# Performance work log

Hardware: AMD Instinct MI355X
Metric: run time of the kernel (lower is better)

## Reference

```python
import jax, jax.numpy as jnp
import numpy as np
import math

B, S, E, H = 4, 1024, 1024, 16
D = E // H


def setup_inputs() -> dict:
    key = jax.random.key(0)
    ks = jax.random.split(key, 10)
    inp = {
        "query": jax.random.normal(ks[0], (B, S, E), dtype=jnp.float32),
        "key": jax.random.normal(ks[1], (B, S, E), dtype=jnp.float32),
        "value": jax.random.normal(ks[2], (B, S, E), dtype=jnp.float32),
        "attn_mask": jax.random.randint(ks[3], (B * H, S, S), 0, 2).astype(bool),
        "key_padding_mask": jax.random.randint(ks[4], (B, S), 0, 2).astype(bool),
        # nn.Linear(E, E, bias=False) weights, stored [out, in] as in torch
        "Wq": jax.random.normal(ks[5], (E, E), dtype=jnp.float32) * 0.02,
        "Wk": jax.random.normal(ks[6], (E, E), dtype=jnp.float32) * 0.02,
        "Wv": jax.random.normal(ks[7], (E, E), dtype=jnp.float32) * 0.02,
        "Wo": jax.random.normal(ks[8], (E, E), dtype=jnp.float32) * 0.02,
    }
    return inp


def reference(query, key, value, attn_mask, key_padding_mask, Wq, Wk, Wv, Wo):
    # projections: torch Linear => x @ W.T; split heads -> [B,H,S,D]
    Q = (query @ Wq.T).reshape(B, S, H, D).transpose(0, 2, 1, 3)
    K = (key @ Wk.T).reshape(B, S, H, D).transpose(0, 2, 1, 3)
    V = (value @ Wv.T).reshape(B, S, H, D).transpose(0, 2, 1, 3)

    scores = jnp.einsum('bhid,bhkd->bhik', Q, K) / math.sqrt(D)  # [B,H,S,S]

    am = attn_mask.reshape(B, H, S, S)
    kpm = jnp.broadcast_to(key_padding_mask[:, None, None, :], (B, H, S, S))
    mask = am | kpm

    # faithful quirks: masked scores set to 0 (not -inf); softmax over dim=2
    # (the QUERY axis i of [b,h,i,k]); masked weights zeroed after softmax.
    scores = jnp.where(mask, 0.0, scores)
    weights = jax.nn.softmax(scores, axis=2)
    weights = jnp.where(mask, 0.0, weights)

    attn = jnp.einsum('bhij,bhjk->bhik', weights, V)  # [B,H,S,D]
    attn = attn.transpose(0, 2, 1, 3).reshape(B, S, H * D)
    return attn @ Wo.T
```

## Files before the change

### kernel.cpp

```cpp
#include <hip/hip_runtime.h>
#include <stdint.h>

#define S_ 1024
#define E_ 1024
#define H_ 16
#define D_ 64
#define BH_ 64

typedef __attribute__((ext_vector_type(4))) float f32x4;
typedef __attribute__((ext_vector_type(8))) _Float16 f16x8;

__device__ __forceinline__ void gl_lds16(const void* g, void* l) {
  __builtin_amdgcn_global_load_lds((__attribute__((address_space(1))) void*)(g),
                                   (__attribute__((address_space(3))) void*)(l), 16, 0, 0);
}

__global__ __launch_bounds__(256) void cvt_f16(const float* __restrict__ q,
                                               const float* __restrict__ k,
                                               const float* __restrict__ v,
                                               const float* __restrict__ wq,
                                               const float* __restrict__ wk,
                                               const float* __restrict__ wv,
                                               const float* __restrict__ wo,
                                               _Float16* __restrict__ dst) {
  size_t i = ((size_t)blockIdx.x * 256 + threadIdx.x) * 4;
  const size_t M4 = 4u << 20, M1 = 1u << 20;
  const float* src;
  size_t off;
  if (i < M4) { src = q; off = i; }
  else if (i < 2 * M4) { src = k; off = i - M4; }
  else if (i < 3 * M4) { src = v; off = i - 2 * M4; }
  else if (i < 3 * M4 + M1) { src = wq; off = i - 3 * M4; }
  else if (i < 3 * M4 + 2 * M1) { src = wk; off = i - (3 * M4 + M1); }
  else if (i < 3 * M4 + 3 * M1) { src = wv; off = i - (3 * M4 + 2 * M1); }
  else { src = wo; off = i - (3 * M4 + 3 * M1); }
  float4 f = *reinterpret_cast<const float4*>(src + off);
  _Float16 h[4];
  h[0] = (_Float16)f.x; h[1] = (_Float16)f.y; h[2] = (_Float16)f.z; h[3] = (_Float16)f.w;
  *reinterpret_cast<uint2*>(dst + i) = *reinterpret_cast<uint2*>(h);
}

__global__ __launch_bounds__(256) void pack_mask(const int* __restrict__ am,
                                                 const int* __restrict__ kpm,
                                                 uint32_t* __restrict__ mw) {
  size_t t = (size_t)blockIdx.x * 256 + threadIdx.x;
  size_t f = t * 4;
  int k = (int)(f & (S_ - 1));
  int b = (int)(f >> 24);
  int4 a = *reinterpret_cast<const int4*>(am + f);
  int4 kp = *reinterpret_cast<const int4*>(kpm + (size_t)b * S_ + k);
  uint32_t nib = (uint32_t)((a.x | kp.x) != 0) | ((uint32_t)((a.y | kp.y) != 0) << 1) |
                 ((uint32_t)((a.z | kp.z) != 0) << 2) | ((uint32_t)((a.w | kp.w) != 0) << 3);
  uint32_t v = nib << ((threadIdx.x & 7) * 4);
  v |= __shfl_xor(v, 1);
  v |= __shfl_xor(v, 2);
  v |= __shfl_xor(v, 4);
  if ((threadIdx.x & 7) == 0) mw[t >> 3] = v;
}

__global__ __launch_bounds__(256) void gemm_proj(const _Float16* __restrict__ qkv,
                                                 const _Float16* __restrict__ wts,
                                                 _Float16* __restrict__ QKo,
                                                 _Float16* __restrict__ Vt) {
  const int K = 1024, BM = 128, BK = 32;
  __shared__ __align__(16) _Float16 As[BM * BK];
  __shared__ __align__(16) _Float16 Bs[BM * BK];
  const int tid = threadIdx.x, wave = tid >> 6, lane = tid & 63;
  const int l15 = lane & 15, lk = lane >> 4;
  const int wr = wave >> 1, wc = wave & 1;
  const int mb = blockIdx.x, nb = blockIdx.y, z = blockIdx.z;
  const _Float16* A = qkv + (size_t)z * (4u << 20);
  const _Float16* Bw = wts + (size_t)z * (1u << 20);
  const int srow = (lane >> 2);
  const int scol = (lane & 3) * 8;
  f32x4 acc[4][4] = {};
  for (int kt = 0; kt < K / BK; ++kt) {
#pragma unroll
    for (int c = 0; c < 2; ++c) {
      int ch = wave * 2 + c;
      int row = ch * 16 + srow;
      gl_lds16(&A[(size_t)(mb * BM + row) * K + kt * BK + scol], &As[ch * 512]);
      gl_lds16(&Bw[(size_t)(nb * BM + row) * K + kt * BK + scol], &Bs[ch * 512]);
    }
    __syncthreads();
    f16x8 a[4], b[4];
#pragma unroll
    for (int m = 0; m < 4; ++m)
      a[m] = *reinterpret_cast<const f16x8*>(&As[(wr * 64 + m * 16 + l15) * BK + lk * 8]);
#pragma unroll
    for (int n = 0; n < 4; ++n)
      b[n] = *reinterpret_cast<const f16x8*>(&Bs[(wc * 64 + n * 16 + l15) * BK + lk * 8]);
#pragma unroll
    for (int m = 0; m < 4; ++m)
#pragma unroll
      for (int n = 0; n < 4; ++n)
        acc[m][n] = __builtin_amdgcn_mfma_f32_16x16x32_f16(a[m], b[n], acc[m][n], 0, 0, 0);
    __syncthreads();
  }
  const float qs = (z == 0) ? 0.125f : 1.0f;
#pragma unroll
  for (int m = 0; m < 4; ++m) {
#pragma unroll
    for (int n = 0; n < 4; ++n) {
#pragma unroll
      for (int r = 0; r < 4; ++r) {
        int gm = mb * BM + wr * 64 + m * 16 + lk * 4 + r;
        int gn = nb * BM + wc * 64 + n * 16 + l15;
        int bb = gm >> 10, s = gm & 1023, h = gn >> 6, d = gn & 63;
        int bh = bb * 16 + h;
        _Float16 v = (_Float16)(acc[m][n][r] * qs);
        if (z == 2)
          Vt[((size_t)bh * D_ + d) * S_ + s] = v;
        else
          QKo[(size_t)z * (4u << 20) + ((size_t)bh * S_ + s) * D_ + d] = v;
      }
    }
  }
}

__global__ __launch_bounds__(256) void attn_denom(const _Float16* __restrict__ Qh,
                                                  const _Float16* __restrict__ Kh,
                                                  const uint32_t* __restrict__ mw,
                                                  float* __restrict__ denom) {
  const int TI = 128, TK = 128, LD = 72;
  __shared__ __align__(16) _Float16 Qs[TI * LD];
  __shared__ __align__(16) _Float16 Ks[TK * LD];
  __shared__ uint32_t Ms[TI * 4];
  __shared__ float red[4][64];
  const int tid = threadIdx.x, wave = tid >> 6, lane = tid & 63;
  const int l15 = lane & 15, lk = lane >> 4;
  const int wr = wave >> 1, wc = wave & 1;
  const int bh = blockIdx.y, kb = blockIdx.x;
  const _Float16* Qb = Qh + (size_t)bh * S_ * D_;
  const _Float16* Kb = Kh + (size_t)bh * S_ * D_;
  const uint32_t* mrow = mw + (size_t)bh * S_ * 32;
#pragma unroll
  for (int j = 0; j < 4; ++j) {
    int c = tid + j * 256;
    int row = c >> 3, c8 = c & 7;
    *reinterpret_cast<uint4*>(&Ks[row * LD + c8 * 8]) =
        *reinterpret_cast<const uint4*>(&Kb[(size_t)(kb * TK + row) * D_ + c8 * 8]);
  }
  float csum[4] = {0.f, 0.f, 0.f, 0.f};
  for (int ib = 0; ib < S_ / TI; ++ib) {
    __syncthreads();
#pragma unroll
    for (int j = 0; j < 4; ++j) {
      int c = tid + j * 256;
      int row = c >> 3, c8 = c & 7;
      *reinterpret_cast<uint4*>(&Qs[row * LD + c8 * 8]) =
          *reinterpret_cast<const uint4*>(&Qb[(size_t)(ib * TI + row) * D_ + c8 * 8]);
    }
    Ms[tid] = mrow[(size_t)(ib * TI + (tid >> 2)) * 32 + kb * 4 + (tid & 3)];
    Ms[tid + 256] = mrow[(size_t)(ib * TI + 64 + (tid >> 2)) * 32 + kb * 4 + (tid & 3)];
    __syncthreads();
    f32x4 acc[4][4] = {};
#pragma unroll
    for (int kk = 0; kk < 2; ++kk) {
      f16x8 a[4], b[4];
#pragma unroll
      for (int m = 0; m < 4; ++m)
        a[m] = *reinterpret_cast<const f16x8*>(&Qs[(wr * 64 + m * 16 + l15) * LD + kk * 32 + lk * 8]);
#pragma unroll
      for (int n = 0; n < 4; ++n)
        b[n] = *reinterpret_cast<const f16x8*>(&Ks[(wc * 64 + n * 16 + l15) * LD + kk * 32 + lk * 8]);
#pragma unroll
      for (int m = 0; m < 4; ++m)
#pragma unroll
        for (int n = 0; n < 4; ++n)
          acc[m][n] = __builtin_amdgcn_mfma_f32_16x16x32_f16(a[m], b[n], acc[m][n], 0, 0, 0);
    }
#pragma unroll
    for (int n = 0; n < 4; ++n) {
      int kcol = wc * 64 + n * 16 + l15;
      int kwl = kcol >> 5;
      int kbit = kcol & 31;
      float part = 0.f;
#pragma unroll
      for (int m = 0; m < 4; ++m) {
        int lr0 = wr * 64 + m * 16 + lk * 4;
#pragma unroll
        for (int r = 0; r < 4; ++r) {
          bool msk = (Ms[(lr0 + r) * 4 + kwl] >> kbit) & 1;
          float e = __expf(acc[m][n][r]);
          part += msk ? 1.0f : e;
        }
      }
      csum[n] += part;
    }
  }
#pragma unroll
  for (int n = 0; n < 4; ++n) {
    float v = csum[n];
    v += __shfl_xor(v, 16);
    v += __shfl_xor(v, 32);
    csum[n] = v;
  }
  __syncthreads();
  if (lane < 16) {
#pragma unroll
    for (int n = 0; n < 4; ++n) red[wave][n * 16 + l15] = csum[n];
  }
  __syncthreads();
  if (tid < 128) {
    int wcx = tid >> 6, col = tid & 63;
    denom[(size_t)bh * S_ + kb * TK + wcx * 64 + col] = red[wcx][col] + red[wcx + 2][col];
  }
}

__global__ __launch_bounds__(256) void vscale(_Float16* __restrict__ Vt,
                                              const float* __restrict__ Dn) {
  size_t e = ((size_t)blockIdx.x * 256 + threadIdx.x) * 8;
  int bh = (int)(e >> 16);
  int s = (int)(e & (S_ - 1));
  uint4 raw = *reinterpret_cast<uint4*>(Vt + e);
  _Float16* h = reinterpret_cast<_Float16*>(&raw);
  const float* dp = Dn + (size_t)bh * S_ + s;
#pragma unroll
  for (int j = 0; j < 8; ++j) h[j] = (_Float16)((float)h[j] / dp[j]);
  *reinterpret_cast<uint4*>(Vt + e) = raw;
}

__global__ __launch_bounds__(256) void attn_pv(const _Float16* __restrict__ Qh,
                                               const _Float16* __restrict__ Kh,
                                               const _Float16* __restrict__ Vp,
                                               const uint32_t* __restrict__ mw,
                                               _Float16* __restrict__ An) {
  const int TI = 128, TK = 128, LD = 72, LW = 136;
  __shared__ __align__(16) _Float16 Qs[TI * LD];
  __shared__ __align__(16) _Float16 Ks[TK * LD];
  __shared__ __align__(16) _Float16 Ws[TI * LW];
  __shared__ uint32_t Ms[TI * 4];
  const int tid = threadIdx.x, wave = tid >> 6, lane = tid & 63;
  const int l15 = lane & 15, lk = lane >> 4;
  const int wr = wave >> 1, wc = wave & 1;
  const int bh = blockIdx.y, ib = blockIdx.x;
  const _Float16* Qb = Qh + (size_t)bh * S_ * D_;
  const _Float16* Kb = Kh + (size_t)bh * S_ * D_;
  const _Float16* Vb = Vp + ((size_t)bh << 16);
  const uint32_t* mrow = mw + (size_t)bh * S_ * 32;
#pragma unroll
  for (int j = 0; j < 4; ++j) {
    int c = tid + j * 256;
    int row = c >> 3, c8 = c & 7;
    *reinterpret_cast<uint4*>(&Qs[row * LD + c8 * 8]) =
        *reinterpret_cast<const uint4*>(&Qb[(size_t)(ib * TI + row) * D_ + c8 * 8]);
  }
  f32x4 acc2[4][2] = {};
  for (int kt = 0; kt < S_ / TK; ++kt) {
    __syncthreads();
#pragma unroll
    for (int j = 0; j < 4; ++j) {
      int c = tid + j * 256;
      int row = c >> 3, c8 = c & 7;
      *reinterpret_cast<uint4*>(&Ks[row * LD + c8 * 8]) =
          *reinterpret_cast<const uint4*>(&Kb[(size_t)(kt * TK + row) * D_ + c8 * 8]);
    }
    Ms[tid] = mrow[(size_t)(ib * TI + (tid >> 2)) * 32 + kt * 4 + (tid & 3)];
    Ms[tid + 256] = mrow[(size_t)(ib * TI + 64 + (tid >> 2)) * 32 + kt * 4 + (tid & 3)];
    __syncthreads();
    f32x4 acc[4][4] = {};
#pragma unroll
    for (int kk = 0; kk < 2; ++kk) {
      f16x8 a[4], b[4];
#pragma unroll
      for (int m = 0; m < 4; ++m)
        a[m] = *reinterpret_cast<const f16x8*>(&Qs[(wr * 64 + m * 16 + l15) * LD + kk * 32 + lk * 8]);
#pragma unroll
      for (int n = 0; n < 4; ++n)
        b[n] = *reinterpret_cast<const f16x8*>(&Ks[(wc * 64 + n * 16 + l15) * LD + kk * 32 + lk * 8]);
#pragma unroll
      for (int m = 0; m < 4; ++m)
#pragma unroll
        for (int n = 0; n < 4; ++n)
          acc[m][n] = __builtin_amdgcn_mfma_f32_16x16x32_f16(a[m], b[n], acc[m][n], 0, 0, 0);
    }
#pragma unroll
    for (int n = 0; n < 4; ++n) {
      int kcol = wc * 64 + n * 16 + l15;
      int kwl = kcol >> 5;
      int kbit = kcol & 31;
#pragma unroll
      for (int m = 0; m < 4; ++m) {
        int lr0 = wr * 64 + m * 16 + lk * 4;
#pragma unroll
        for (int r = 0; r < 4; ++r) {
          bool msk = (Ms[(lr0 + r) * 4 + kwl] >> kbit) & 1;
          float e = __expf(acc[m][n][r]);
          Ws[(lr0 + r) * LW + kcol] = msk ? (_Float16)0.f : (_Float16)e;
        }
      }
    }
    __syncthreads();
#pragma unroll
    for (int kk = 0; kk < 4; ++kk) {
      f16x8 a2[4], b2[2];
#pragma unroll
      for (int m = 0; m < 4; ++m)
        a2[m] = *reinterpret_cast<const f16x8*>(&Ws[(wr * 64 + m * 16 + l15) * LW + kk * 32 + lk * 8]);
#pragma unroll
      for (int n = 0; n < 2; ++n)
        b2[n] = *reinterpret_cast<const f16x8*>(
            &Vb[(size_t)(wc * 32 + n * 16 + l15) * S_ + kt * TK + kk * 32 + lk * 8]);
#pragma unroll
      for (int m = 0; m < 4; ++m)
#pragma unroll
        for (int n = 0; n < 2; ++n)
          acc2[m][n] = __builtin_amdgcn_mfma_f32_16x16x32_f16(a2[m], b2[n], acc2[m][n], 0, 0, 0);
    }
  }
  const int b_ = bh >> 4, h = bh & 15;
#pragma unroll
  for (int m = 0; m < 4; ++m) {
#pragma unroll
    for (int n = 0; n < 2; ++n) {
#pragma unroll
      for (int r = 0; r < 4; ++r) {
        int i = ib * TI + wr * 64 + m * 16 + lk * 4 + r;
        int d = wc * 32 + n * 16 + l15;
        An[((size_t)(b_ * S_ + i)) * E_ + h * D_ + d] = (_Float16)acc2[m][n][r];
      }
    }
  }
}

__global__ __launch_bounds__(256) void gemm_out(const _Float16* __restrict__ An,
                                               const _Float16* __restrict__ Bw,
                                               float* __restrict__ outp) {
  const int K = 1024, BM = 128, BN = 64, BK = 32;
  __shared__ __align__(16) _Float16 As[BM * BK];
  __shared__ __align__(16) _Float16 Bs[BN * BK];
  const int tid = threadIdx.x, wave = tid >> 6, lane = tid & 63;
  const int l15 = lane & 15, lk = lane >> 4;
  const int wr = wave >> 1, wc = wave & 1;
  const int mb = blockIdx.x, nb = blockIdx.y;
  const int srow = (lane >> 2), scol = (lane & 3) * 8;
  f32x4 acc[4][2] = {};
  for (int kt = 0; kt < K / BK; ++kt) {
#pragma unroll
    for (int c = 0; c < 2; ++c) {
      int ch = wave * 2 + c;
      int row = ch * 16 + srow;
      gl_lds16(&An[(size_t)(mb * BM + row) * K + kt * BK + scol], &As[ch * 512]);
    }
    {
      int row = wave * 16 + srow;
      gl_lds16(&Bw[(size_t)(nb * BN + row) * K + kt * BK + scol], &Bs[wave * 512]);
    }
    __syncthreads();
    f16x8 a[4], b[2];
#pragma unroll
    for (int m = 0; m < 4; ++m)
      a[m] = *reinterpret_cast<const f16x8*>(&As[(wr * 64 + m * 16 + l15) * BK + lk * 8]);
#pragma unroll
    for (int n = 0; n < 2; ++n)
      b[n] = *reinterpret_cast<const f16x8*>(&Bs[(wc * 32 + n * 16 + l15) * BK + lk * 8]);
#pragma unroll
    for (int m = 0; m < 4; ++m)
#pragma unroll
      for (int n = 0; n < 2; ++n)
        acc[m][n] = __builtin_amdgcn_mfma_f32_16x16x32_f16(a[m], b[n], acc[m][n], 0, 0, 0);
    __syncthreads();
  }
#pragma unroll
  for (int m = 0; m < 4; ++m) {
#pragma unroll
    for (int n = 0; n < 2; ++n) {
#pragma unroll
      for (int r = 0; r < 4; ++r) {
        int gm = mb * BM + wr * 64 + m * 16 + lk * 4 + r;
        int gn = nb * BN + wc * 32 + n * 16 + l15;
        outp[(size_t)gm * 1024 + gn] = acc[m][n][r];
      }
    }
  }
}

extern "C" void kernel_launch(void* const* d_in, const int* in_sizes, int n_in,
                              void* d_out, int out_size, void* d_ws, size_t ws_size,
                              hipStream_t stream) {
  const float* q = (const float*)d_in[0];
  const float* k = (const float*)d_in[1];
  const float* v = (const float*)d_in[2];
  const int* am = (const int*)d_in[3];
  const int* kpm = (const int*)d_in[4];
  const float* Wq = (const float*)d_in[5];
  const float* Wk = (const float*)d_in[6];
  const float* Wv = (const float*)d_in[7];
  const float* Wo = (const float*)d_in[8];
  float* out = (float*)d_out;

  _Float16* cvt = (_Float16*)d_ws;
  _Float16* qkv = cvt;
  _Float16* wts = cvt + (12u << 20);
  _Float16* wob = cvt + (15u << 20);
  uint8_t* ws = (uint8_t*)d_ws;
  _Float16* Qh = (_Float16*)(ws + (32ull << 20));
  _Float16* Kh = (_Float16*)(ws + (40ull << 20));
  _Float16* Vt = (_Float16*)(ws + (48ull << 20));
  uint32_t* MW = (uint32_t*)(ws + (56ull << 20));
  float* Dn = (float*)(ws + (64ull << 20));
  _Float16* An = qkv;

  cvt_f16<<<16384, 256, 0, stream>>>(q, k, v, Wq, Wk, Wv, Wo, cvt);
  pack_mask<<<65536, 256, 0, stream>>>(am, kpm, MW);
  gemm_proj<<<dim3(32, 8, 3), 256, 0, stream>>>(qkv, wts, Qh, Vt);
  attn_denom<<<dim3(8, 64), 256, 0, stream>>>(Qh, Kh, MW, Dn);
  vscale<<<2048, 256, 0, stream>>>(Vt, Dn);
  attn_pv<<<dim3(8, 64), 256, 0, stream>>>(Qh, Kh, Vt, MW, An);
  gemm_out<<<dim3(32, 16), 256, 0, stream>>>(An, wob, out);
}
```

Baseline: 565.4 us.

## Fuse V scaling into denom kernel, transpose V via LDS, retile output GEMM

The V-projection epilogue now stages its tile in shared memory so the transposed V is written with coalesced 16-byte stores instead of scattered 2-byte ones. The separate vscale kernel is removed: attn_denom computes reciprocal denominators and scales its own column slice of Vt in place, which drops a launch and the Dn buffer. attn_pv prefetches the V fragments from global memory before the barrier so the load latency overlaps the score computation. gemm_out moves to 128x128 tiles, halving the grid and raising per-block reuse at the cost of more accumulator registers.

```diff
diff --git a/kernel.cpp b/kernel.cpp
--- a/kernel.cpp
+++ b/kernel.cpp
@@ -65,6 +65,7 @@
   const int K = 1024, BM = 128, BK = 32;
   __shared__ __align__(16) _Float16 As[BM * BK];
   __shared__ __align__(16) _Float16 Bs[BM * BK];
+  __shared__ __align__(16) _Float16 Ts[64 * 136];
   const int tid = threadIdx.x, wave = tid >> 6, lane = tid & 63;
   const int l15 = lane & 15, lk = lane >> 4;
   const int wr = wave >> 1, wc = wave & 1;
@@ -97,22 +98,45 @@
         acc[m][n] = __builtin_amdgcn_mfma_f32_16x16x32_f16(a[m], b[n], acc[m][n], 0, 0, 0);
     __syncthreads();
   }
-  const float qs = (z == 0) ? 0.125f : 1.0f;
-#pragma unroll
-  for (int m = 0; m < 4; ++m) {
-#pragma unroll
-    for (int n = 0; n < 4; ++n) {
-#pragma unroll
-      for (int r = 0; r < 4; ++r) {
-        int gm = mb * BM + wr * 64 + m * 16 + lk * 4 + r;
-        int gn = nb * BM + wc * 64 + n * 16 + l15;
-        int bb = gm >> 10, s = gm & 1023, h = gn >> 6, d = gn & 63;
-        int bh = bb * 16 + h;
-        _Float16 v = (_Float16)(acc[m][n][r] * qs);
-        if (z == 2)
-          Vt[((size_t)bh * D_ + d) * S_ + s] = v;
-        else
-          QKo[(size_t)z * (4u << 20) + ((size_t)bh * S_ + s) * D_ + d] = v;
+  if (z == 2) {
+    const int bb = mb >> 3, s0 = (mb & 7) * 128;
+    for (int hh = 0; hh < 2; ++hh) {
+      __syncthreads();
+      if (wc == hh) {
+#pragma unroll
+        for (int m = 0; m < 4; ++m)
+#pragma unroll
+          for (int n = 0; n < 4; ++n)
+#pragma unroll
+            for (int r = 0; r < 4; ++r)
+              Ts[(n * 16 + l15) * 136 + wr * 64 + m * 16 + lk * 4 + r] =
+                  (_Float16)acc[m][n][r];
+      }
+      __syncthreads();
+      int bh = bb * 16 + nb * 2 + hh;
+#pragma unroll
+      for (int u = 0; u < 4; ++u) {
+        int c = tid + u * 256;
+        int d = c >> 4, seg = c & 15;
+        *reinterpret_cast<uint4*>(&Vt[(((size_t)bh * 64 + d) << 10) + s0 + seg * 8]) =
+            *reinterpret_cast<const uint4*>(&Ts[d * 136 + seg * 8]);
+      }
+    }
+  } else {
+    const float qs = (z == 0) ? 0.125f : 1.0f;
+#pragma unroll
+    for (int m = 0; m < 4; ++m) {
+#pragma unroll
+      for (int n = 0; n < 4; ++n) {
+#pragma unroll
+        for (int r = 0; r < 4; ++r) {
+          int gm = mb * BM + wr * 64 + m * 16 + lk * 4 + r;
+          int gn = nb * BM + wc * 64 + n * 16 + l15;
+          int bb = gm >> 10, s = gm & 1023, h = gn >> 6, d = gn & 63;
+          int bh = bb * 16 + h;
+          QKo[(size_t)z * (4u << 20) + ((size_t)bh * S_ + s) * D_ + d] =
+              (_Float16)(acc[m][n][r] * qs);
+        }
       }
     }
   }
@@ -121,12 +145,13 @@
 __global__ __launch_bounds__(256) void attn_denom(const _Float16* __restrict__ Qh,
                                                   const _Float16* __restrict__ Kh,
                                                   const uint32_t* __restrict__ mw,
-                                                  float* __restrict__ denom) {
+                                                  _Float16* __restrict__ Vt) {
   const int TI = 128, TK = 128, LD = 72;
   __shared__ __align__(16) _Float16 Qs[TI * LD];
   __shared__ __align__(16) _Float16 Ks[TK * LD];
   __shared__ uint32_t Ms[TI * 4];
   __shared__ float red[4][64];
+  __shared__ float dv[128];
   const int tid = threadIdx.x, wave = tid >> 6, lane = tid & 63;
   const int l15 = lane & 15, lk = lane >> 4;
   const int wr = wave >> 1, wc = wave & 1;
@@ -202,23 +227,20 @@
     for (int n = 0; n < 4; ++n) red[wave][n * 16 + l15] = csum[n];
   }
   __syncthreads();
-  if (tid < 128) {
-    int wcx = tid >> 6, col = tid & 63;
-    denom[(size_t)bh * S_ + kb * TK + wcx * 64 + col] = red[wcx][col] + red[wcx + 2][col];
-  }
-}
-
-__global__ __launch_bounds__(256) void vscale(_Float16* __restrict__ Vt,
-                                              const float* __restrict__ Dn) {
-  size_t e = ((size_t)blockIdx.x * 256 + threadIdx.x) * 8;
-  int bh = (int)(e >> 16);
-  int s = (int)(e & (S_ - 1));
-  uint4 raw = *reinterpret_cast<uint4*>(Vt + e);
-  _Float16* h = reinterpret_cast<_Float16*>(&raw);
-  const float* dp = Dn + (size_t)bh * S_ + s;
-#pragma unroll
-  for (int j = 0; j < 8; ++j) h[j] = (_Float16)((float)h[j] / dp[j]);
-  *reinterpret_cast<uint4*>(Vt + e) = raw;
+  if (tid < 128) dv[tid] = 1.0f / (red[tid >> 6][tid & 63] + red[(tid >> 6) + 2][tid & 63]);
+  __syncthreads();
+  _Float16* Vblk = Vt + ((size_t)bh << 16) + kb * TK;
+#pragma unroll
+  for (int u = 0; u < 4; ++u) {
+    int c = tid + u * 256;
+    int d = c >> 4, k8 = (c & 15) * 8;
+    _Float16* p = Vblk + (size_t)d * 1024 + k8;
+    uint4 raw = *reinterpret_cast<uint4*>(p);
+    _Float16* h = reinterpret_cast<_Float16*>(&raw);
+#pragma unroll
+    for (int j = 0; j < 8; ++j) h[j] = (_Float16)((float)h[j] * dv[k8 + j]);
+    *reinterpret_cast<uint4*>(p) = raw;
+  }
 }
 
 __global__ __launch_bounds__(256) void attn_pv(const _Float16* __restrict__ Qh,
@@ -248,6 +270,13 @@
   }
   f32x4 acc2[4][2] = {};
   for (int kt = 0; kt < S_ / TK; ++kt) {
+    f16x8 vpre[4][2];
+#pragma unroll
+    for (int kk = 0; kk < 4; ++kk)
+#pragma unroll
+      for (int n = 0; n < 2; ++n)
+        vpre[kk][n] = *reinterpret_cast<const f16x8*>(
+            &Vb[(size_t)(wc * 32 + n * 16 + l15) * S_ + kt * TK + kk * 32 + lk * 8]);
     __syncthreads();
 #pragma unroll
     for (int j = 0; j < 4; ++j) {
@@ -294,19 +323,15 @@
     __syncthreads();
 #pragma unroll
     for (int kk = 0; kk < 4; ++kk) {
-      f16x8 a2[4], b2[2];
+      f16x8 a2[4];
 #pragma unroll
       for (int m = 0; m < 4; ++m)
         a2[m] = *reinterpret_cast<const f16x8*>(&Ws[(wr * 64 + m * 16 + l15) * LW + kk * 32 + lk * 8]);
 #pragma unroll
-      for (int n = 0; n < 2; ++n)
-        b2[n] = *reinterpret_cast<const f16x8*>(
-            &Vb[(size_t)(wc * 32 + n * 16 + l15) * S_ + kt * TK + kk * 32 + lk * 8]);
-#pragma unroll
       for (int m = 0; m < 4; ++m)
 #pragma unroll
         for (int n = 0; n < 2; ++n)
-          acc2[m][n] = __builtin_amdgcn_mfma_f32_16x16x32_f16(a2[m], b2[n], acc2[m][n], 0, 0, 0);
+          acc2[m][n] = __builtin_amdgcn_mfma_f32_16x16x32_f16(a2[m], vpre[kk][n], acc2[m][n], 0, 0, 0);
     }
   }
   const int b_ = bh >> 4, h = bh & 15;
@@ -327,49 +352,46 @@
 __global__ __launch_bounds__(256) void gemm_out(const _Float16* __restrict__ An,
                                                const _Float16* __restrict__ Bw,
                                                float* __restrict__ outp) {
-  const int K = 1024, BM = 128, BN = 64, BK = 32;
+  const int K = 1024, BM = 128, BK = 32;
   __shared__ __align__(16) _Float16 As[BM * BK];
-  __shared__ __align__(16) _Float16 Bs[BN * BK];
+  __shared__ __align__(16) _Float16 Bs[BM * BK];
   const int tid = threadIdx.x, wave = tid >> 6, lane = tid & 63;
   const int l15 = lane & 15, lk = lane >> 4;
   const int wr = wave >> 1, wc = wave & 1;
   const int mb = blockIdx.x, nb = blockIdx.y;
   const int srow = (lane >> 2), scol = (lane & 3) * 8;
-  f32x4 acc[4][2] = {};
+  f32x4 acc[4][4] = {};
   for (int kt = 0; kt < K / BK; ++kt) {
 #pragma unroll
     for (int c = 0; c < 2; ++c) {
       int ch = wave * 2 + c;
       int row = ch * 16 + srow;
       gl_lds16(&An[(size_t)(mb * BM + row) * K + kt * BK + scol], &As[ch * 512]);
-    }
-    {
-      int row = wave * 16 + srow;
-      gl_lds16(&Bw[(size_t)(nb * BN + row) * K + kt * BK + scol], &Bs[wave * 512]);
-    }
-    __syncthreads();
-    f16x8 a[4], b[2];
+      gl_lds16(&Bw[(size_t)(nb * BM + row) * K + kt * BK + scol], &Bs[ch * 512]);
+    }
+    __syncthreads();
+    f16x8 a[4], b[4];
 #pragma unroll
     for (int m = 0; m < 4; ++m)
       a[m] = *reinterpret_cast<const f16x8*>(&As[(wr * 64 + m * 16 + l15) * BK + lk * 8]);
 #pragma unroll
-    for (int n = 0; n < 2; ++n)
-      b[n] = *reinterpret_cast<const f16x8*>(&Bs[(wc * 32 + n * 16 + l15) * BK + lk * 8]);
+    for (int n = 0; n < 4; ++n)
+      b[n] = *reinterpret_cast<const f16x8*>(&Bs[(wc * 64 + n * 16 + l15) * BK + lk * 8]);
 #pragma unroll
     for (int m = 0; m < 4; ++m)
 #pragma unroll
-      for (int n = 0; n < 2; ++n)
+      for (int n = 0; n < 4; ++n)
         acc[m][n] = __builtin_amdgcn_mfma_f32_16x16x32_f16(a[m], b[n], acc[m][n], 0, 0, 0);
     __syncthreads();
   }
 #pragma unroll
   for (int m = 0; m < 4; ++m) {
 #pragma unroll
-    for (int n = 0; n < 2; ++n) {
+    for (int n = 0; n < 4; ++n) {
 #pragma unroll
       for (int r = 0; r < 4; ++r) {
         int gm = mb * BM + wr * 64 + m * 16 + lk * 4 + r;
-        int gn = nb * BN + wc * 32 + n * 16 + l15;
+        int gn = nb * BM + wc * 64 + n * 16 + l15;
         outp[(size_t)gm * 1024 + gn] = acc[m][n][r];
       }
     }
@@ -399,14 +421,12 @@
   _Float16* Kh = (_Float16*)(ws + (40ull << 20));
   _Float16* Vt = (_Float16*)(ws + (48ull << 20));
   uint32_t* MW = (uint32_t*)(ws + (56ull << 20));
-  float* Dn = (float*)(ws + (64ull << 20));
   _Float16* An = qkv;
 
   cvt_f16<<<16384, 256, 0, stream>>>(q, k, v, Wq, Wk, Wv, Wo, cvt);
   pack_mask<<<65536, 256, 0, stream>>>(am, kpm, MW);
   gemm_proj<<<dim3(32, 8, 3), 256, 0, stream>>>(qkv, wts, Qh, Vt);
-  attn_denom<<<dim3(8, 64), 256, 0, stream>>>(Qh, Kh, MW, Dn);
-  vscale<<<2048, 256, 0, stream>>>(Vt, Dn);
+  attn_denom<<<dim3(8, 64), 256, 0, stream>>>(Qh, Kh, MW, Vt);
   attn_pv<<<dim3(8, 64), 256, 0, stream>>>(Qh, Kh, Vt, MW, An);
-  gemm_out<<<dim3(32, 16), 256, 0, stream>>>(An, wob, out);
-}
+  gemm_out<<<dim3(32, 8), 256, 0, stream>>>(An, wob, out);
+}
```

Result: no change. 562.2 us (-0.6%).
